# Optimization experiments

Measured on AMD Instinct MI355X. Metric: run time of the kernel, lower is better.

Reference implementation:

```python
import jax, jax.numpy as jnp
import numpy as np

L, B, E, H, HID = 2048, 4, 512, 8, 2048
HD = E // H


def setup_inputs() -> dict:
    key = jax.random.key(0)
    ks = jax.random.split(key, 6)
    s = 0.02
    x = jax.random.normal(ks[0], (L, B, E), jnp.float32)
    in_proj_w = jax.random.normal(ks[1], (3 * E, E), jnp.float32) * s
    in_proj_b = jnp.zeros((3 * E,), jnp.float32)
    out_w = jax.random.normal(ks[2], (E, E), jnp.float32) * s
    out_b = jnp.zeros((E,), jnp.float32)
    w1 = jax.random.normal(ks[3], (HID, E), jnp.float32) * s  # torch Linear: (out, in)
    b1 = jnp.zeros((HID,), jnp.float32)
    w2 = jax.random.normal(ks[4], (E, HID), jnp.float32) * s
    b2 = jnp.zeros((E,), jnp.float32)
    ln_g = jnp.ones((E,), jnp.float32)
    ln_b = jnp.zeros((E,), jnp.float32)
    return {"x": x, "in_proj_w": in_proj_w, "in_proj_b": in_proj_b,
            "out_w": out_w, "out_b": out_b, "w1": w1, "b1": b1,
            "w2": w2, "b2": b2, "ln_g": ln_g, "ln_b": ln_b}


def _pos_encoding(S, Emb, dtype):
    # even i: sin((t+1) * 10000^(-i/E)); odd i: cos((t+1) * 10000^(-(i+1)/E))
    t = jnp.arange(S, dtype=dtype)[:, None]
    i = jnp.arange(Emb, dtype=dtype)[None, :]
    even = jnp.sin((t + 1.0) * jnp.power(10000.0, -i / Emb))
    odd = jnp.cos((t + 1.0) * jnp.power(10000.0, -(i + 1.0) / Emb))
    return jnp.where(jnp.arange(Emb)[None, :] % 2 == 0, even, odd)  # (S, Emb)


def _layernorm(x, g, b, eps=1e-5):
    mu = jnp.mean(x, axis=-1, keepdims=True)
    var = jnp.mean(jnp.square(x - mu), axis=-1, keepdims=True)
    return (x - mu) * jax.lax.rsqrt(var + eps) * g + b


def _mha(x, in_proj_w, in_proj_b, out_w, out_b):
    # x: (L, B, E); self-attention, torch MultiheadAttention semantics
    qkv = jnp.einsum('lbe,fe->lbf', x, in_proj_w) + in_proj_b
    q, k, v = jnp.split(qkv, 3, axis=-1)
    q = q.reshape(L, B, H, HD)
    k = k.reshape(L, B, H, HD)
    v = v.reshape(L, B, H, HD)
    scores = jnp.einsum('lbhd,mbhd->bhlm', q, k) / np.sqrt(HD).astype(np.float32)
    attn = jax.nn.softmax(scores, axis=-1)
    o = jnp.einsum('bhlm,mbhd->lbhd', attn, v).reshape(L, B, E)
    return jnp.einsum('lbe,fe->lbf', o, out_w) + out_b


def reference(x, in_proj_w, in_proj_b, out_w, out_b, w1, b1, w2, b2, ln_g, ln_b):
    # positional encoding: varies along dim1, broadcasts along dim0 (as in source)
    pe = _pos_encoding(x.shape[1], x.shape[2], x.dtype)  # (B, E)
    x = x + pe[None, :, :]
    # Post-Norm path
    x = _layernorm(_mha(x, in_proj_w, in_proj_b, out_w, out_b) + x, ln_g, ln_b)
    h = jax.nn.gelu(jnp.einsum('lbe,he->lbh', x, w1) + b1, approximate=False)
    ff = jnp.einsum('lbh,eh->lbe', h, w2) + b2
    x = _layernorm(ff + x, ln_g, ln_b)
    return x
```

## Files before the change

### kernel.cpp

```cpp
#include <hip/hip_runtime.h>

typedef unsigned short u16;
typedef unsigned int   u32;
typedef u16  u16x2 __attribute__((ext_vector_type(2)));
typedef u16  u16x4 __attribute__((ext_vector_type(4)));
typedef u16  u16x8 __attribute__((ext_vector_type(8)));
typedef short s8v  __attribute__((ext_vector_type(8)));
typedef float f4v  __attribute__((ext_vector_type(4)));
typedef u32  u32x2 __attribute__((ext_vector_type(2)));
typedef u32  u32x4 __attribute__((ext_vector_type(4)));

#define L_SEQ 2048
#define B_SZ  4
#define E_DIM 512
#define H_CNT 8
#define HD    64
#define HID   2048
#define M_ROWS (L_SEQ * B_SZ)
#define QSCALE 0.18033688011112042f

__device__ __forceinline__ u16 f2b(float f) {
    unsigned u = __builtin_bit_cast(unsigned, f);
    u += 0x7fffu + ((u >> 16) & 1u);
    return (u16)(u >> 16);
}
__device__ __forceinline__ float b2f(u16 u) {
    u32 x = ((u32)u) << 16; return __builtin_bit_cast(float, x);
}
#if defined(__has_builtin)
#if __has_builtin(__builtin_amdgcn_cvt_pk_bf16_f32)
#define HAVE_PK_BF16 1
#endif
#if __has_builtin(__builtin_amdgcn_rcpf)
#define HAVE_RCPF 1
#endif
#endif
__device__ __forceinline__ u32 pk_trunc(float a, float b) {
#ifdef HAVE_PK_BF16
    typedef __bf16 bf2 __attribute__((ext_vector_type(2)));
    bf2 r = __builtin_amdgcn_cvt_pk_bf16_f32(a, b);
    return __builtin_bit_cast(u32, r);
#else
    u32 ua = __builtin_bit_cast(u32, a), ub = __builtin_bit_cast(u32, b);
    return (ua >> 16) | (ub & 0xffff0000u);
#endif
}
__device__ __forceinline__ float frcp(float x) {
#ifdef HAVE_RCPF
    return __builtin_amdgcn_rcpf(x);
#else
    return 1.0f / x;
#endif
}
__device__ __forceinline__ void gload_lds16(const u16* g, u16* l) {
    __builtin_amdgcn_global_load_lds((__attribute__((address_space(1))) void*)(u16*)g,
                                     (__attribute__((address_space(3))) void*)l, 16, 0, 0);
}
__device__ __forceinline__ float gelu_f(float v) {
    float y2 = v * (1.5957691216f + 0.0713548576f * v * v);
    return v / (1.0f + __expf(-y2));
}

__global__ __launch_bounds__(256) void pe_tab_k(float* __restrict__ pet) {
    int i = blockIdx.x * 256 + threadIdx.x;
    int e = i & (E_DIM - 1);
    float t = (float)(i >> 9) + 1.0f;
    int ee = (e & 1) ? (e + 1) : e;
    float w = exp2f((-(float)ee / 512.0f) * 13.287712379549449f);
    pet[i] = (e & 1) ? cosf(t * w) : sinf(t * w);
}

__global__ __launch_bounds__(256) void pe_add_k(const float* __restrict__ x,
                                                const float* __restrict__ pet,
                                                u16* __restrict__ xpb) {
    int idx = (blockIdx.x * 256 + threadIdx.x) * 4;
    f4v v = *(const f4v*)(x + idx);
    f4v p = *(const f4v*)(pet + (idx & 2047));
    u16x4 o;
#pragma unroll
    for (int i = 0; i < 4; ++i) o[i] = f2b(v[i] + p[i]);
    *(u16x4*)(xpb + idx) = o;
}

__global__ __launch_bounds__(256) void conv4_k(const float* __restrict__ s1, u16* __restrict__ d1, int n1,
                                               const float* __restrict__ s2, u16* __restrict__ d2, int n2,
                                               const float* __restrict__ s3, u16* __restrict__ d3, int n3,
                                               const float* __restrict__ s4, u16* __restrict__ d4) {
    int o = (blockIdx.x * 256 + threadIdx.x) * 4;
    const float* s; u16* d;
    if (o < n1) { s = s1; d = d1; }
    else { o -= n1;
        if (o < n2) { s = s2; d = d2; }
        else { o -= n2;
            if (o < n3) { s = s3; d = d3; }
            else { o -= n3; s = s4; d = d4; } } }
    f4v v = *(const f4v*)(s + o);
    u16x4 q;
#pragma unroll
    for (int i = 0; i < 4; ++i) q[i] = f2b(v[i]);
    *(u16x4*)(d + o) = q;
}

template <int NP, bool WRITEF, bool WRITEB>
__global__ __launch_bounds__(256)
void ln_c(const u16* __restrict__ p0, const u16* __restrict__ p1,
          const u16* __restrict__ p2, const u16* __restrict__ p3,
          const float* __restrict__ bias, const u16* __restrict__ resid,
          const float* __restrict__ gw, const float* __restrict__ bw,
          float* __restrict__ outF, u16* __restrict__ outB) {
    int wave = threadIdx.x >> 6, lane = threadIdx.x & 63;
    size_t row = (size_t)blockIdx.x * 4 + wave;
    size_t off = row * E_DIM + lane * 8;
    u16x8 rv = *(const u16x8*)(resid + off);
    f4v a, b;
#pragma unroll
    for (int i = 0; i < 4; ++i) { a[i] = b2f(rv[i]); b[i] = b2f(rv[i + 4]); }
    a += *(const f4v*)(bias + lane * 8);
    b += *(const f4v*)(bias + lane * 8 + 4);
    const u16* ps[4] = {p0, p1, p2, p3};
#pragma unroll
    for (int z = 0; z < NP; ++z) {
        u16x8 t = *(const u16x8*)(ps[z] + off);
#pragma unroll
        for (int i = 0; i < 4; ++i) { a[i] += b2f(t[i]); b[i] += b2f(t[i + 4]); }
    }
    float s = (a[0] + a[1]) + (a[2] + a[3]) + (b[0] + b[1]) + (b[2] + b[3]);
#pragma unroll
    for (int o = 1; o < 64; o <<= 1) s += __shfl_xor(s, o, 64);
    float mu = s * (1.0f / E_DIM);
    float q = 0.f;
#pragma unroll
    for (int i = 0; i < 4; ++i) { float d = a[i] - mu; q += d * d; }
#pragma unroll
    for (int i = 0; i < 4; ++i) { float d = b[i] - mu; q += d * d; }
#pragma unroll
    for (int o = 1; o < 64; o <<= 1) q += __shfl_xor(q, o, 64);
    float rstd = rsqrtf(q * (1.0f / E_DIM) + 1e-5f);
    f4v g0 = *(const f4v*)(gw + lane * 8), g1 = *(const f4v*)(gw + lane * 8 + 4);
    f4v w0 = *(const f4v*)(bw + lane * 8), w1 = *(const f4v*)(bw + lane * 8 + 4);
    f4v y0, y1;
#pragma unroll
    for (int i = 0; i < 4; ++i) { y0[i] = (a[i] - mu) * rstd * g0[i] + w0[i];
                                  y1[i] = (b[i] - mu) * rstd * g1[i] + w1[i]; }
    if (WRITEF) {
        *(f4v*)(outF + off)     = y0;
        *(f4v*)(outF + off + 4) = y1;
    }
    if (WRITEB) {
        u16x8 o;
#pragma unroll
        for (int i = 0; i < 4; ++i) { o[i] = f2b(y0[i]); o[i + 4] = f2b(y1[i]); }
        *(u16x8*)(outB + off) = o;
    }
}

__global__ __launch_bounds__(256) void transpose_v_k(const u16* __restrict__ vb,
                                                     u16* __restrict__ vt) {
    __shared__ __align__(16) u16 T[64 * 66];
    int t = threadIdx.x;
    int lt = blockIdx.x, bh = blockIdx.y;
    const u16* src = vb + (size_t)bh * (L_SEQ * HD) + (size_t)lt * 64 * HD;
    int lr = t >> 2, d0 = (t & 3) * 16;
    s8v va = *(const s8v*)(src + lr * HD + d0);
    s8v vb8 = *(const s8v*)(src + lr * HD + d0 + 8);
#pragma unroll
    for (int c = 0; c < 4; ++c) {
        u16x2 p0; p0[0] = (u16)va[c * 2]; p0[1] = (u16)va[c * 2 + 1];
        u16x2 p1; p1[0] = (u16)vb8[c * 2]; p1[1] = (u16)vb8[c * 2 + 1];
        *(u16x2*)(&T[lr * 66 + d0 + c * 2])     = p0;
        *(u16x2*)(&T[lr * 66 + d0 + 8 + c * 2]) = p1;
    }
    __syncthreads();
    int d = t >> 2, l0 = (t & 3) * 16;
    u16 tmp[16];
#pragma unroll
    for (int i = 0; i < 16; ++i) tmp[i] = T[(l0 + i) * 66 + d];
    u16* dst = vt + (size_t)bh * (L_SEQ * HD) + (size_t)d * L_SEQ + lt * 64 + l0;
    u16x8 o0, o1;
#pragma unroll
    for (int i = 0; i < 8; ++i) { o0[i] = tmp[i]; o1[i] = tmp[8 + i]; }
    *(u16x8*)dst       = o0;
    *(u16x8*)(dst + 8) = o1;
}

__global__ __launch_bounds__(256, 4)
void gemm_ks(const u16* __restrict__ A, const u16* __restrict__ Bw,
             int N, int K, int Kper,
             u16* __restrict__ q0, u16* __restrict__ q1) {
    __shared__ __align__(16) u16 As[2][128 * 32];
    __shared__ __align__(16) u16 Bs[2][128 * 32];
    const int tid = threadIdx.x;
    const int wave = tid >> 6, lane = tid & 63;
    const int col = lane & 15, quad = lane >> 4;
    const int n = blockIdx.x;
    const int xcd = n & 7, loc = n >> 3;
    const int bn = (loc & 3) * 128;
    const int bm = (xcd * 8 + ((loc >> 2) & 7)) * 128;
    const int kz = loc >> 5;
    u16* pz = kz ? q1 : q0;
    const int wm = (wave >> 1) * 64, wn = (wave & 1) * 64;
    f4v acc[4][4] = {};
    const int srow = wave * 16 + (lane >> 2);
    const int soff = (lane & 3) * 8;
    const u16* Ag = A + (size_t)(bm + srow) * K + kz * Kper + soff;
    const u16* Bg = Bw + (size_t)(bn + srow) * K + kz * Kper + soff;
    const int wo = wave * 512;
    gload_lds16(Ag,                  &As[0][wo]);
    gload_lds16(Ag + (size_t)64 * K, &As[0][wo + 2048]);
    gload_lds16(Bg,                  &Bs[0][wo]);
    gload_lds16(Bg + (size_t)64 * K, &Bs[0][wo + 2048]);
    const int nit = Kper >> 5;
    for (int t = 0; t < nit; ++t) {
        const int cur = t & 1, nxt = cur ^ 1;
        __syncthreads();
        if (t + 1 < nit) {
            const int kc = (t + 1) * 32;
            gload_lds16(Ag + kc,                  &As[nxt][wo]);
            gload_lds16(Ag + (size_t)64 * K + kc, &As[nxt][wo + 2048]);
            gload_lds16(Bg + kc,                  &Bs[nxt][wo]);
            gload_lds16(Bg + (size_t)64 * K + kc, &Bs[nxt][wo + 2048]);
        }
        s8v af[4], bf[4];
#pragma unroll
        for (int i = 0; i < 4; ++i) af[i] = *(const s8v*)(&As[cur][(wm + i * 16 + col) * 32 + quad * 8]);
#pragma unroll
        for (int j = 0; j < 4; ++j) bf[j] = *(const s8v*)(&Bs[cur][(wn + j * 16 + col) * 32 + quad * 8]);
#pragma unroll
        for (int i = 0; i < 4; ++i)
#pragma unroll
            for (int j = 0; j < 4; ++j)
                acc[i][j] = __builtin_amdgcn_mfma_f32_16x16x32_bf16(af[i], bf[j], acc[i][j], 0, 0, 0);
    }
#pragma unroll
    for (int j = 0; j < 4; ++j) {
        int gn = bn + wn + j * 16 + col;
#pragma unroll
        for (int i = 0; i < 4; ++i) {
            int m0 = bm + wm + i * 16 + quad * 4;
#pragma unroll
            for (int r = 0; r < 4; ++r)
                pz[(size_t)(m0 + r) * N + gn] = f2b(acc[i][j][r]);
        }
    }
}

#define G8_STAGE(Ad, Bd, kf)                                                           \
    {                                                                                  \
        _Pragma("unroll")                                                              \
        for (int s = 0; s < 2; ++s) {                                                  \
            const int q = (s * 8 + wave) * 64 + lane;                                  \
            const int rho = q >> 2;                                                    \
            gload_lds16(A  + (size_t)(bm + rho) * Ka + (kf) + gsw, (Ad) + q * 8);      \
            gload_lds16(Bw + (size_t)(bn + rho) * Kb + (kf) + gsw, (Bd) + q * 8);      \
        }                                                                              \
    }

#define G8_COMPUTE(Ab_, Bb_)                                                           \
    {                                                                                  \
        s8v bfr[4];                                                                    \
        _Pragma("unroll")                                                              \
        for (int j = 0; j < 4; ++j) {                                                  \
            const int rB = wc * 64 + j * 16 + col;                                     \
            bfr[j] = *(const s8v*)((Bb_) + rB * 32 + ((quad ^ ((rB >> 1) & 3)) * 8));  \
        }                                                                              \
        _Pragma("unroll")                                                              \
        for (int ih = 0; ih < 2; ++ih) {                                               \
            s8v afr[4];                                                                \
            _Pragma("unroll")                                                          \
            for (int i = 0; i < 4; ++i) {                                              \
                const int rA = wr * 128 + (ih * 4 + i) * 16 + col;                     \
                afr[i] = *(const s8v*)((Ab_) + rA * 32 + ((quad ^ ((rA >> 1) & 3)) * 8)); \
            }                                                                          \
            __builtin_amdgcn_s_setprio(1);                                             \
            _Pragma("unroll")                                                          \
            for (int i = 0; i < 4; ++i)                                                \
                _Pragma("unroll")                                                      \
                for (int j = 0; j < 4; ++j)                                            \
                    acc[ih * 4 + i][j] = __builtin_amdgcn_mfma_f32_16x16x32_bf16(afr[i], bfr[j], acc[ih * 4 + i][j], 0, 0, 0); \
            __builtin_amdgcn_s_setprio(0);                                             \
        }                                                                              \
    }

template <int MODE, int NTL>
__global__ __launch_bounds__(512, 2)
void gemm8(const u16* __restrict__ A, const u16* __restrict__ Bw,
           const float* __restrict__ bias, int Ka, int Kb, int N,
           u16* __restrict__ o0, u16* __restrict__ o1, u16* __restrict__ o2) {
    extern __shared__ __align__(16) u16 LDS[];
    const int tid = threadIdx.x;
    const int wave = tid >> 6, lane = tid & 63;
    const int col = lane & 15, quad = lane >> 4;
    const int wr = wave >> 2, wc = wave & 3;
    const int n = blockIdx.x;
    const int xcd = n & 7, loc = n >> 3;
    const int mt = xcd * 4 + (loc & 3);
    const int nt = loc >> 2;
    const int bm = mt * 256, bn = nt * 256;
    const int gsw = ((lane & 3) ^ ((lane >> 3) & 3)) * 8;
    f4v acc[8][4] = {};
    u16* A0 = LDS;          u16* B0 = LDS + 8192;
    u16* A1 = LDS + 16384;  u16* B1 = LDS + 24576;
    u16* A2 = LDS + 32768;  u16* B2 = LDS + 40960;
    G8_STAGE(A0, B0, 0);
    G8_STAGE(A1, B1, 32);
    asm volatile("s_waitcnt vmcnt(4)" ::: "memory");
    __builtin_amdgcn_s_barrier();
    __builtin_amdgcn_sched_barrier(0);
    for (int t = 0; t < 14; ++t) {
        G8_STAGE(A2, B2, (t + 2) * 32);
        G8_COMPUTE(A0, B0);
        asm volatile("s_waitcnt vmcnt(4)" ::: "memory");
        __builtin_amdgcn_s_barrier();
        __builtin_amdgcn_sched_barrier(0);
        u16* ta = A0; A0 = A1; A1 = A2; A2 = ta;
        u16* tb = B0; B0 = B1; B1 = B2; B2 = tb;
    }
    G8_COMPUTE(A0, B0);
    asm volatile("s_waitcnt vmcnt(0)" ::: "memory");
    __builtin_amdgcn_s_barrier();
    __builtin_amdgcn_sched_barrier(0);
    G8_COMPUTE(A1, B1);
#pragma unroll
    for (int j = 0; j < 4; ++j) {
        const int gn = bn + wc * 64 + j * 16 + col;
        const float bv = bias[gn];
        if (MODE == 0) {
            const int which = gn >> 9, hh = (gn >> 6) & 7, d = gn & 63;
            u16* dst = (which == 0) ? o0 : (which == 1) ? o1 : o2;
            const float qs = (which == 0) ? QSCALE : 1.0f;
#pragma unroll
            for (int i = 0; i < 8; ++i) {
                const int m0 = bm + wr * 128 + i * 16 + quad * 4;
#pragma unroll
                for (int r = 0; r < 4; ++r) {
                    const int m = m0 + r;
                    const int l = m >> 2, bb = m & 3;
                    dst[((size_t)(bb * H_CNT + hh) * L_SEQ + l) * HD + d] = f2b((acc[i][j][r] + bv) * qs);
                }
            }
        } else {
#pragma unroll
            for (int i = 0; i < 8; ++i) {
                const int m0 = bm + wr * 128 + i * 16 + quad * 4;
#pragma unroll
                for (int r = 0; r < 4; ++r)
                    o0[(size_t)(m0 + r) * N + gn] = f2b(gelu_f(acc[i][j][r] + bv));
            }
        }
    }
}

__global__ __launch_bounds__(512, 4)
void attn_k(const u16* __restrict__ qg, const u16* __restrict__ kg,
            const u16* __restrict__ vtg, u16* __restrict__ og) {
    __shared__ __align__(16) u16 KV[2][2][2][2][64 * 32];
    __shared__ float LSB[2][256];
    const int tid = threadIdx.x;
    const int wave = tid >> 6, lane = tid & 63;
    const int grp = wave >> 2, w4 = wave & 3;
    const int col = lane & 15, quad = lane >> 4;
    const int flat = blockIdx.x;
    const int xcd = flat & 7, loc = flat >> 3;
    const int bh = xcd * 4 + (loc >> 4);
    const int qc = loc & 15;
    const size_t base = (size_t)bh * (L_SEQ * HD);
    s8v qf[2][2];
#pragma unroll
    for (int t = 0; t < 2; ++t) {
        const int qrow = qc * 128 + w4 * 32 + t * 16 + col;
#pragma unroll
        for (int hh = 0; hh < 2; ++hh)
            qf[t][hh] = *(const s8v*)(qg + base + (size_t)qrow * HD + hh * 32 + quad * 8);
    }
    f4v oa[2][4] = {};
    float ls0 = 0.f, ls1 = 0.f;
    const int h = w4 & 1, r0 = (w4 >> 1) * 16;
    const int srow = lane >> 2, c = lane & 3;
    const int cp = c ^ ((srow >> 1) & 3);
    const int sig = ((srow >> 2) << 3) + ((r0 >> 4) << 2) + (srow & 3);
    const u16* Kg = kg + base + (size_t)(sig + grp * 1024) * HD + h * 32 + cp * 8;
    const u16* Vg = vtg + base + (size_t)(r0 + srow) * L_SEQ + grp * 1024 + h * 32 + cp * 8;
    {
        gload_lds16(Kg,                      &KV[grp][0][0][h][r0 * 32]);
        gload_lds16(Kg + (size_t)32 * HD,    &KV[grp][0][0][h][(r0 + 32) * 32]);
        gload_lds16(Vg,                      &KV[grp][1][0][h][r0 * 32]);
        gload_lds16(Vg + (size_t)32 * L_SEQ, &KV[grp][1][0][h][(r0 + 32) * 32]);
    }
    const int perm = (col >> 1) & 3;
    for (int it = 0; it < 16; ++it) {
        const int cur = it & 1, nxt = cur ^ 1;
        __syncthreads();
        if (it + 1 < 16) {
            const int kv0 = (it + 1) * 64;
            gload_lds16(Kg + (size_t)kv0 * HD,         &KV[grp][0][nxt][h][r0 * 32]);
            gload_lds16(Kg + (size_t)(kv0 + 32) * HD,  &KV[grp][0][nxt][h][(r0 + 32) * 32]);
            gload_lds16(Vg + kv0,                      &KV[grp][1][nxt][h][r0 * 32]);
            gload_lds16(Vg + kv0 + (size_t)32 * L_SEQ, &KV[grp][1][nxt][h][(r0 + 32) * 32]);
        }
        f4v st[2][4];
#pragma unroll
        for (int j = 0; j < 4; ++j) {
            s8v k0 = *(const s8v*)(&KV[grp][0][cur][0][(j * 16 + col) * 32 + ((quad ^ perm) * 8)]);
            s8v k1 = *(const s8v*)(&KV[grp][0][cur][1][(j * 16 + col) * 32 + ((quad ^ perm) * 8)]);
#pragma unroll
            for (int t = 0; t < 2; ++t) {
                f4v z = {};
                z = __builtin_amdgcn_mfma_f32_16x16x32_bf16(k0, qf[t][0], z, 0, 0, 0);
                z = __builtin_amdgcn_mfma_f32_16x16x32_bf16(k1, qf[t][1], z, 0, 0, 0);
                st[t][j] = z;
            }
        }
        u32 pk[2][4][2];
#pragma unroll
        for (int t = 0; t < 2; ++t)
#pragma unroll
            for (int j = 0; j < 4; ++j) {
                f4v p;
#pragma unroll
                for (int r = 0; r < 4; ++r) p[r] = __builtin_amdgcn_exp2f(st[t][j][r]);
                float psum = (p[0] + p[1]) + (p[2] + p[3]);
                if (t == 0) ls0 += psum; else ls1 += psum;
                pk[t][j][0] = pk_trunc(p[0], p[1]);
                pk[t][j][1] = pk_trunc(p[2], p[3]);
            }
#pragma unroll
        for (int c2 = 0; c2 < 2; ++c2) {
            s8v pf[2];
#pragma unroll
            for (int t = 0; t < 2; ++t) {
                u32x4 q4 = {pk[t][2 * c2][0], pk[t][2 * c2][1],
                            pk[t][2 * c2 + 1][0], pk[t][2 * c2 + 1][1]};
                pf[t] = __builtin_bit_cast(s8v, q4);
            }
#pragma unroll
            for (int dj = 0; dj < 4; ++dj) {
                s8v vf = *(const s8v*)(&KV[grp][1][cur][c2][(dj * 16 + col) * 32 + ((quad ^ perm) * 8)]);
#pragma unroll
                for (int t = 0; t < 2; ++t)
                    oa[t][dj] = __builtin_amdgcn_mfma_f32_16x16x32_bf16(pf[t], vf, oa[t][dj], 0, 0, 0);
            }
        }
    }
    ls0 += __shfl_xor(ls0, 16, 64); ls0 += __shfl_xor(ls0, 32, 64);
    ls1 += __shfl_xor(ls1, 16, 64); ls1 += __shfl_xor(ls1, 32, 64);
    float* cmb = (float*)&KV[1][0][0][0][0];
    const int slot = w4 * 64 + lane;
    if (grp == 1) {
#pragma unroll
        for (int t = 0; t < 2; ++t)
#pragma unroll
            for (int dj = 0; dj < 4; ++dj)
                *(f4v*)(cmb + ((size_t)(t * 4 + dj) * 256 + slot) * 4) = oa[t][dj];
        LSB[0][slot] = ls0;
        LSB[1][slot] = ls1;
    }
    __syncthreads();
    if (grp == 0) {
#pragma unroll
        for (int t = 0; t < 2; ++t)
#pragma unroll
            for (int dj = 0; dj < 4; ++dj)
                oa[t][dj] += *(const f4v*)(cmb + ((size_t)(t * 4 + dj) * 256 + slot) * 4);
        ls0 += LSB[0][slot];
        ls1 += LSB[1][slot];
        const int b = bh >> 3, hd = bh & 7;
#pragma unroll
        for (int t = 0; t < 2; ++t)
#pragma unroll
            for (int r = 0; r < 4; ++r) {
                float lv = __shfl(t == 0 ? ls0 : ls1, quad * 4 + r, 64);
                float inv = frcp(lv);
                int lrow = qc * 128 + w4 * 32 + t * 16 + quad * 4 + r;
                size_t mrow = (size_t)(lrow * 4 + b) * E_DIM + hd * HD;
#pragma unroll
                for (int dj = 0; dj < 4; ++dj)
                    og[mrow + dj * 16 + col] = f2b(oa[t][dj][r] * inv);
            }
    }
}

extern "C" void kernel_launch(void* const* d_in, const int* in_sizes, int n_in,
                              void* d_out, int out_size, void* d_ws, size_t ws_size,
                              hipStream_t stream) {
    const float* x     = (const float*)d_in[0];
    const float* w_qkv = (const float*)d_in[1];
    const float* b_qkv = (const float*)d_in[2];
    const float* w_out = (const float*)d_in[3];
    const float* b_out = (const float*)d_in[4];
    const float* w1    = (const float*)d_in[5];
    const float* b1    = (const float*)d_in[6];
    const float* w2    = (const float*)d_in[7];
    const float* b2    = (const float*)d_in[8];
    const float* ln_g  = (const float*)d_in[9];
    const float* ln_b  = (const float*)d_in[10];

    char* ws = (char*)d_ws;
    u16*   WQKV = (u16*)(ws + 0);
    u16*   WOUT = (u16*)(ws + 1572864);
    u16*   W1B  = (u16*)(ws + 2097152);
    u16*   W2B  = (u16*)(ws + 4194304);
    u16*   XPB  = (u16*)(ws + 6291456);
    u16*   QB   = (u16*)(ws + 14680064);
    u16*   KB   = (u16*)(ws + 23068672);
    u16*   VB   = (u16*)(ws + 31457280);
    u16*   VT   = (u16*)(ws + 39845888);
    float* PET  = (float*)(ws + 82837504);
    u16*   OB   = VB;
    u16*   OP0  = (u16*)(ws + 48234496);
    u16*   OP1  = (u16*)(ws + 56623104);
    u16*   X3B  = QB;
    u16*   HB   = (u16*)(ws + 48234496);
    u16*   FP0  = XPB;
    u16*   FP1  = KB;

    static bool attr_done = false;
    if (!attr_done) {
        hipFuncSetAttribute((const void*)gemm8<0, 6>,
                            hipFuncAttributeMaxDynamicSharedMemorySize, 98304);
        hipFuncSetAttribute((const void*)gemm8<2, 8>,
                            hipFuncAttributeMaxDynamicSharedMemorySize, 98304);
        attr_done = true;
    }

    pe_tab_k<<<8, 256, 0, stream>>>(PET);
    pe_add_k<<<4096, 256, 0, stream>>>(x, PET, XPB);
    conv4_k<<<3072, 256, 0, stream>>>(w_qkv, WQKV, 3 * E_DIM * E_DIM,
                                      w_out, WOUT, E_DIM * E_DIM,
                                      w1, W1B, HID * E_DIM,
                                      w2, W2B);
    gemm8<0, 6><<<192, 512, 98304, stream>>>(XPB, WQKV, b_qkv, E_DIM, E_DIM, 0,
                                             QB, KB, VB);
    transpose_v_k<<<dim3(32, 32), 256, 0, stream>>>(VB, VT);
    attn_k<<<512, 512, 0, stream>>>(QB, KB, VT, OB);
    gemm_ks<<<512, 256, 0, stream>>>(OB, WOUT, E_DIM, E_DIM, 256, OP0, OP1);
    ln_c<2, false, true><<<2048, 256, 0, stream>>>(OP0, OP1, nullptr, nullptr,
                                                   b_out, XPB, ln_g, ln_b, nullptr, X3B);
    gemm8<2, 8><<<256, 512, 98304, stream>>>(X3B, W1B, b1, E_DIM, E_DIM, HID,
                                             HB, nullptr, nullptr);
    gemm_ks<<<512, 256, 0, stream>>>(HB, W2B, E_DIM, HID, 1024, FP0, FP1);
    ln_c<2, true, false><<<2048, 256, 0, stream>>>(FP0, FP1, nullptr, nullptr,
                                                   b2, X3B, ln_g, ln_b, (float*)d_out, nullptr);
}
```

Before: 239.3 us.

## Add 256x128-tile GEMM kernel for QKV projection and split-K FFN2

Adds a new g28 GEMM template that uses 256x128 output tiles with a triple-buffered LDS pipeline and two blocks per CU. It replaces the QKV projection, going from 192 to 384 blocks, and the second FFN GEMM, which now uses 2-way split-K with partial outputs instead of gemm_ks. The aim is more blocks and better occupancy on the mid-size GEMMs. The cost is less data reuse per tile, and the split-K path adds extra partial-output memory traffic.

```diff
diff --git a/kernel.cpp b/kernel.cpp
--- a/kernel.cpp
+++ b/kernel.cpp
@@ -324,13 +324,105 @@
     for (int j = 0; j < 4; ++j) {
         const int gn = bn + wc * 64 + j * 16 + col;
         const float bv = bias[gn];
+#pragma unroll
+        for (int i = 0; i < 8; ++i) {
+            const int m0 = bm + wr * 128 + i * 16 + quad * 4;
+#pragma unroll
+            for (int r = 0; r < 4; ++r)
+                o0[(size_t)(m0 + r) * N + gn] = f2b(gelu_f(acc[i][j][r] + bv));
+        }
+    }
+}
+
+#define G28_STAGE(Ad, Bd, kf)                                                          \
+    {                                                                                  \
+        _Pragma("unroll")                                                              \
+        for (int s = 0; s < 2; ++s) {                                                  \
+            const int qa = s * 512 + tid;                                              \
+            const int rhoA = qa >> 2;                                                  \
+            gload_lds16(A + (size_t)(bm + rhoA) * Ka + koff + (kf) + gsw, (Ad) + qa * 8); \
+        }                                                                              \
+        {                                                                              \
+            const int rhoB = tid >> 2;                                                 \
+            gload_lds16(Bw + (size_t)(bn + rhoB) * Kb + koff + (kf) + gsw, (Bd) + tid * 8); \
+        }                                                                              \
+    }
+
+#define G28_COMPUTE(Ab_, Bb_)                                                          \
+    {                                                                                  \
+        s8v bfr[4], afr[4];                                                            \
+        _Pragma("unroll")                                                              \
+        for (int j = 0; j < 4; ++j) {                                                  \
+            const int rB = wc * 64 + j * 16 + col;                                     \
+            bfr[j] = *(const s8v*)((Bb_) + rB * 32 + ((quad ^ ((rB >> 1) & 3)) * 8));  \
+        }                                                                              \
+        _Pragma("unroll")                                                              \
+        for (int i = 0; i < 4; ++i) {                                                  \
+            const int rA = wr * 64 + i * 16 + col;                                     \
+            afr[i] = *(const s8v*)((Ab_) + rA * 32 + ((quad ^ ((rA >> 1) & 3)) * 8));  \
+        }                                                                              \
+        __builtin_amdgcn_s_setprio(1);                                                 \
+        _Pragma("unroll")                                                              \
+        for (int i = 0; i < 4; ++i)                                                    \
+            _Pragma("unroll")                                                          \
+            for (int j = 0; j < 4; ++j)                                                \
+                acc[i][j] = __builtin_amdgcn_mfma_f32_16x16x32_bf16(afr[i], bfr[j], acc[i][j], 0, 0, 0); \
+        __builtin_amdgcn_s_setprio(0);                                                 \
+    }
+
+template <int MODE, int NTL, int KZL, int KTILES>
+__global__ __launch_bounds__(512, 2)
+void g28(const u16* __restrict__ A, const u16* __restrict__ Bw,
+         const float* __restrict__ bias, int Ka, int Kb, int N,
+         u16* __restrict__ o0, u16* __restrict__ o1, u16* __restrict__ o2) {
+    extern __shared__ __align__(16) u16 LDS[];
+    const int tid = threadIdx.x;
+    const int wave = tid >> 6, lane = tid & 63;
+    const int col = lane & 15, quad = lane >> 4;
+    const int wr = wave >> 1, wc = wave & 1;
+    const int n = blockIdx.x;
+    const int xcd = n & 7, loc = n >> 3;
+    const int mt = xcd * 4 + (loc & 3);
+    const int rest = loc >> 2;
+    const int nt = (NTL == 1) ? 0 : (rest % NTL);
+    const int kz = (KZL == 1) ? 0 : (rest / NTL);
+    const int bm = mt * 256, bn = nt * 128;
+    const int koff = kz * (KTILES * 32);
+    const int gsw = ((lane & 3) ^ ((lane >> 3) & 3)) * 8;
+    f4v acc[4][4] = {};
+    u16* A0 = LDS;          u16* B0 = LDS + 8192;
+    u16* A1 = LDS + 12288;  u16* B1 = LDS + 20480;
+    u16* A2 = LDS + 24576;  u16* B2 = LDS + 32768;
+    G28_STAGE(A0, B0, 0);
+    G28_STAGE(A1, B1, 32);
+    asm volatile("s_waitcnt vmcnt(3)" ::: "memory");
+    __builtin_amdgcn_s_barrier();
+    __builtin_amdgcn_sched_barrier(0);
+    for (int t = 0; t < KTILES - 2; ++t) {
+        G28_STAGE(A2, B2, (t + 2) * 32);
+        G28_COMPUTE(A0, B0);
+        asm volatile("s_waitcnt vmcnt(3)" ::: "memory");
+        __builtin_amdgcn_s_barrier();
+        __builtin_amdgcn_sched_barrier(0);
+        u16* ta = A0; A0 = A1; A1 = A2; A2 = ta;
+        u16* tb = B0; B0 = B1; B1 = B2; B2 = tb;
+    }
+    G28_COMPUTE(A0, B0);
+    asm volatile("s_waitcnt vmcnt(0)" ::: "memory");
+    __builtin_amdgcn_s_barrier();
+    __builtin_amdgcn_sched_barrier(0);
+    G28_COMPUTE(A1, B1);
+#pragma unroll
+    for (int j = 0; j < 4; ++j) {
+        const int gn = bn + wc * 64 + j * 16 + col;
         if (MODE == 0) {
+            const float bv = bias[gn];
             const int which = gn >> 9, hh = (gn >> 6) & 7, d = gn & 63;
             u16* dst = (which == 0) ? o0 : (which == 1) ? o1 : o2;
             const float qs = (which == 0) ? QSCALE : 1.0f;
 #pragma unroll
-            for (int i = 0; i < 8; ++i) {
-                const int m0 = bm + wr * 128 + i * 16 + quad * 4;
+            for (int i = 0; i < 4; ++i) {
+                const int m0 = bm + wr * 64 + i * 16 + quad * 4;
 #pragma unroll
                 for (int r = 0; r < 4; ++r) {
                     const int m = m0 + r;
@@ -339,12 +431,13 @@
                 }
             }
         } else {
-#pragma unroll
-            for (int i = 0; i < 8; ++i) {
-                const int m0 = bm + wr * 128 + i * 16 + quad * 4;
+            u16* pz = (kz == 0) ? o0 : o1;
+#pragma unroll
+            for (int i = 0; i < 4; ++i) {
+                const int m0 = bm + wr * 64 + i * 16 + quad * 4;
 #pragma unroll
                 for (int r = 0; r < 4; ++r)
-                    o0[(size_t)(m0 + r) * N + gn] = f2b(gelu_f(acc[i][j][r] + bv));
+                    pz[(size_t)(m0 + r) * N + gn] = f2b(acc[i][j][r]);
             }
         }
     }
@@ -515,8 +608,10 @@
 
     static bool attr_done = false;
     if (!attr_done) {
-        hipFuncSetAttribute((const void*)gemm8<0, 6>,
-                            hipFuncAttributeMaxDynamicSharedMemorySize, 98304);
+        hipFuncSetAttribute((const void*)g28<0, 12, 1, 16>,
+                            hipFuncAttributeMaxDynamicSharedMemorySize, 73728);
+        hipFuncSetAttribute((const void*)g28<3, 4, 2, 32>,
+                            hipFuncAttributeMaxDynamicSharedMemorySize, 73728);
         hipFuncSetAttribute((const void*)gemm8<2, 8>,
                             hipFuncAttributeMaxDynamicSharedMemorySize, 98304);
         attr_done = true;
@@ -528,8 +623,8 @@
                                       w_out, WOUT, E_DIM * E_DIM,
                                       w1, W1B, HID * E_DIM,
                                       w2, W2B);
-    gemm8<0, 6><<<192, 512, 98304, stream>>>(XPB, WQKV, b_qkv, E_DIM, E_DIM, 0,
-                                             QB, KB, VB);
+    g28<0, 12, 1, 16><<<384, 512, 73728, stream>>>(XPB, WQKV, b_qkv, E_DIM, E_DIM, 0,
+                                                   QB, KB, VB);
     transpose_v_k<<<dim3(32, 32), 256, 0, stream>>>(VB, VT);
     attn_k<<<512, 512, 0, stream>>>(QB, KB, VT, OB);
     gemm_ks<<<512, 256, 0, stream>>>(OB, WOUT, E_DIM, E_DIM, 256, OP0, OP1);
@@ -537,7 +632,8 @@
                                                    b_out, XPB, ln_g, ln_b, nullptr, X3B);
     gemm8<2, 8><<<256, 512, 98304, stream>>>(X3B, W1B, b1, E_DIM, E_DIM, HID,
                                              HB, nullptr, nullptr);
-    gemm_ks<<<512, 256, 0, stream>>>(HB, W2B, E_DIM, HID, 1024, FP0, FP1);
+    g28<3, 4, 2, 32><<<256, 512, 73728, stream>>>(HB, W2B, nullptr, HID, HID, E_DIM,
+                                                  FP0, FP1, nullptr);
     ln_c<2, true, false><<<2048, 256, 0, stream>>>(FP0, FP1, nullptr, nullptr,
                                                    b2, X3B, ln_g, ln_b, (float*)d_out, nullptr);
 }
```

Measured after the change: 232.6 us. -2.8%, faster.
